# Kernel tuning notes

Measured on AMD Instinct MI355X. Metric: run time of the kernel, lower is better.

## Reference

```python
import jax, jax.numpy as jnp
import numpy as np

N_STATES = 32
N_CAMP = 64
DAYS = 365
BATCH = 128
BASIS = 1e-10


def setup_inputs() -> dict:
    key = jax.random.key(0)
    k1, k2, k3 = jax.random.split(key, 3)
    S = N_STATES
    adstock = jax.random.uniform(k1, (BATCH, N_CAMP, DAYS), dtype=jnp.float32)
    mu = jax.random.uniform(k2, ((S - 1) * (S - 1),), dtype=jnp.float32)
    beta = jax.random.uniform(k3, (N_CAMP * (S - 1) * (S - 1),), dtype=jnp.float32)
    return {"adstock": adstock, "mu": mu, "beta": beta}


def _transition(adstock, mu, beta):
    # adstock: [B, C, D]; time T = D - 1 (first day dropped, as in adstock[:, :, 1:])
    S = N_STATES
    B, C, D = adstock.shape
    T = D - 1
    # call() passes -mu into make_transition_matrix
    mu_m = jnp.reshape(-mu, (1, 1, S - 1, S - 1))
    beta_m = jnp.reshape(beta, (C, S - 1, S - 1))
    # tensordot(adstock[b, :, 1:], beta, [0, 0]) for every b -> einsum over camp axis
    O_beta = jnp.einsum('bct,cij->btij', adstock[:, :, 1:], beta_m)  # [B,T,S-1,S-1]
    num = jnp.exp(O_beta + mu_m)
    den = 1.0 + jnp.sum(num, axis=-1, keepdims=True)
    Q_div = num / den                          # [B,T,S-1,S-1] off-diagonal probs
    Q_same = 1.0 - jnp.sum(Q_div, axis=-1)     # [B,T,S-1]    stay probability
    # The TF diag-set loop places, for row i of Q_div: columns j<i stay at j,
    # columns j>=i shift to j+1, and Q_same goes on column i (insert-diagonal).
    i = jnp.arange(S - 1)[:, None]             # [S-1,1]
    j = jnp.arange(S)[None, :]                 # [1,S]
    idx = jnp.clip(jnp.where(j < i, j, j - 1), 0, S - 2)  # [S-1,S]
    gathered = jnp.take_along_axis(Q_div, jnp.broadcast_to(idx, (B, T, S - 1, S)), axis=-1)
    Q_temp = jnp.where(j == i, Q_same[..., None], gathered)  # [B,T,S-1,S]
    # Absorbing last row: basis everywhere, mass 1-(S-1)*basis on last state.
    last = jnp.full((B, T, 1, S), BASIS, dtype=adstock.dtype)
    last = last.at[..., -1].set(1.0 - (S - 1) * BASIS)
    Q = jnp.concatenate([Q_temp, last], axis=2)  # [B,T,S,S]
    return jnp.maximum(Q, BASIS)


def reference(adstock, mu, beta):
    return _transition(adstock, mu, beta)
```

## Files before the change

kernel.cpp:

```cpp
#include <hip/hip_runtime.h>
#include <cstdint>
#include <cstddef>

#define Bb 128
#define Cc 64
#define Dd 365
#define Tt 364
#define Ss 32
#define SM1 31
#define NIJ 961
#define BASISF 1e-10f
#define NBLK 256
#define NUNITS 11648
#define NWAVES 4096

typedef _Float16 f16x8 __attribute__((ext_vector_type(8)));
typedef float f32x4 __attribute__((ext_vector_type(4)));

__global__ void prep_kernel(const float* __restrict__ mu,
                            const float* __restrict__ beta,
                            _Float16* __restrict__ B2,
                            float* __restrict__ emu_perm) {
    int idx = blockIdx.x * blockDim.x + threadIdx.x;
    int m = idx >> 6, c = idx & 63;
    int rem = m & 255;
    int i = (m >> 8) * 8 + (rem >> 6) * 2 + ((rem & 15) >> 3);
    int j = 4 * (rem & 7) + ((rem >> 4) & 3);
    float val = (i < SM1 && j < SM1) ? beta[c * NIJ + i * SM1 + j] : 0.0f;
    B2[((size_t)(c >> 3) * 1024 + m) * 8 + (c & 7)] = (_Float16)val;
    if (idx < 1024) {
        int m2 = idx, rem2 = m2 & 255;
        int i2 = (m2 >> 8) * 8 + (rem2 >> 6) * 2 + ((rem2 & 15) >> 3);
        int j2 = 4 * (rem2 & 7) + ((rem2 >> 4) & 3);
        emu_perm[m2] = (i2 < SM1 && j2 < SM1) ? __expf(-mu[i2 * SM1 + j2]) : 1.0f;
    }
}

template <int CTRL>
__device__ __forceinline__ float dpp_mov(float x) {
    union { float f; int i; } u, v;
    u.f = x;
    v.i = __builtin_amdgcn_update_dpp(0, u.i, CTRL, 0xf, 0xf, true);
    return v.f;
}
template <int CTRL>
__device__ __forceinline__ float dpp_add(float s) { return s + dpp_mov<CTRL>(s); }

__global__ __launch_bounds__(1024, 1)
void transition_persist_kernel(const float* __restrict__ adstock,
                               const _Float16* __restrict__ B2,
                               const float* __restrict__ emu_perm,
                               float* __restrict__ out)
{
    const int tid  = threadIdx.x;
    const int lane = tid & 63;
    const int w    = tid >> 6;
    const int je   = lane & 15;
    const int grp  = lane >> 4;
    const int a     = je & 7;
    const int ihalf = je >> 3;
    const int j0    = 4 * a;

    __shared__ _Float16 Blds[65536];
    __shared__ float emuL[1024];

    #pragma unroll
    for (int s = 0; s < 8; ++s) {
        const int o8 = s * 8192 + tid * 8;
        *reinterpret_cast<f16x8*>(&Blds[o8]) =
            *reinterpret_cast<const f16x8*>(B2 + o8);
    }
    emuL[tid] = emu_perm[tid];
    __syncthreads();

    const float m3 = (a == 7) ? 0.0f : 1.0f;

    const int gw = blockIdx.x * 16 + w;
    const int ub = (int)(((long)NUNITS * gw) / NWAVES);
    const int ue = (int)(((long)NUNITS * (gw + 1)) / NWAVES);

    for (int u = ub; u < ue; ++u) {
        const int chunk = u >> 2;
        const int nq    = u & 3;
        const int bt0   = chunk * 16;

        const int bt = bt0 + je;
        const int b  = bt / Tt, t = bt - b * Tt;
        const float* abase = adstock + ((size_t)b * Cc) * Dd + 1 + t;

        float a0f[8], a1f[8];
        #pragma unroll
        for (int u8 = 0; u8 < 8; ++u8) {
            a0f[u8] = abase[(size_t)(grp * 8 + u8) * Dd];
            a1f[u8] = abase[(size_t)(32 + grp * 8 + u8) * Dd];
        }
        f16x8 a0, a1;
        #pragma unroll
        for (int u8 = 0; u8 < 8; ++u8) {
            a0[u8] = (_Float16)a0f[u8];
            a1[u8] = (_Float16)a1f[u8];
        }

        #pragma unroll
        for (int qp = 0; qp < 4; ++qp) {
            const int colb = nq * 256 + qp * 64 + je;
            f16x8 Bf[8];
            #pragma unroll
            for (int p = 0; p < 4; ++p) {
                Bf[2 * p]     = *reinterpret_cast<const f16x8*>(
                    &Blds[((0 * 4 + grp) * 1024 + colb + p * 16) * 8]);
                Bf[2 * p + 1] = *reinterpret_cast<const f16x8*>(
                    &Blds[((1 * 4 + grp) * 1024 + colb + p * 16) * 8]);
            }

            float emq[4];
            #pragma unroll
            for (int p = 0; p < 4; ++p)
                emq[p] = emuL[nq * 256 + qp * 64 + p * 16 + je];

            f32x4 acc[4];
            #pragma unroll
            for (int p = 0; p < 4; ++p) {
                f32x4 z = {0.f, 0.f, 0.f, 0.f};
                f32x4 t0 = __builtin_amdgcn_mfma_f32_16x16x32_f16(a0, Bf[2 * p], z, 0, 0, 0);
                acc[p] = __builtin_amdgcn_mfma_f32_16x16x32_f16(a1, Bf[2 * p + 1], t0, 0, 0, 0);
            }

            const int i_lane = nq * 8 + 2 * qp + ihalf;
            const size_t obase = (size_t)(bt0 + grp * 4) * 1024
                               + (size_t)i_lane * 32 + j0;

            #pragma unroll
            for (int r = 0; r < 4; ++r) {
                float np[4];
                #pragma unroll
                for (int p = 0; p < 4; ++p) np[p] = __expf(acc[p][r]) * emq[p];

                float s = np[0] + np[1] + fmaf(np[3], m3, np[2]);
                s = dpp_add<0xB1>(s);
                s = dpp_add<0x4E>(s);
                float t1 = dpp_mov<0x124>(s);
                float t2 = dpp_mov<0x12C>(s);
                s += (je & 4) ? t1 : t2;
                const float inv = __builtin_amdgcn_rcpf(1.0f + s);

                const float sh0 = dpp_mov<0x111>(np[3]);
                const float prev[4] = {sh0, np[0], np[1], np[2]};

                float v[4];
                #pragma unroll
                for (int p = 0; p < 4; ++p) {
                    const int j = j0 + p;
                    float x = (j < i_lane) ? np[p] * inv
                            : ((j == i_lane) ? inv : prev[p] * inv);
                    v[p] = fmaxf(x, BASISF);
                }
                if (nq == 3 && qp == 3) {
                    const bool ab = (i_lane == SM1);
                    v[0] = ab ? BASISF : v[0];
                    v[1] = ab ? BASISF : v[1];
                    v[2] = ab ? BASISF : v[2];
                    v[3] = ab ? ((a == 7) ? (1.0f - SM1 * BASISF) : BASISF) : v[3];
                }
                f32x4 vv = {v[0], v[1], v[2], v[3]};
                *reinterpret_cast<f32x4*>(out + obase + (size_t)r * 1024) = vv;
            }
        }
    }
}

__global__ __launch_bounds__(256, 4)
void transition_fallback_kernel(const float* __restrict__ adstock,
                                const float* __restrict__ beta,
                                const float* __restrict__ mu,
                                float* __restrict__ out) {
    const int b  = blockIdx.x;
    const int t0 = blockIdx.y * 16;
    const int tid = threadIdx.x;

    __shared__ float adT[Cc][16];
    __shared__ float num_lds[8][964];

    for (int k = tid; k < Cc * 16; k += 256) {
        int c = k >> 4, tt = k & 15, t = t0 + tt;
        adT[c][tt] = (t < Tt) ? adstock[(size_t)b * (Cc * Dd) + c * Dd + 1 + t] : 0.0f;
    }
    __syncthreads();

    const int ij0 = tid * 4;
    const bool active = (ij0 < 964);
    float acc[16][4];
    #pragma unroll
    for (int tt = 0; tt < 16; ++tt) { acc[tt][0]=0;acc[tt][1]=0;acc[tt][2]=0;acc[tt][3]=0; }

    if (active) {
        for (int c = 0; c < Cc; ++c) {
            const float* bsrc = beta + (size_t)c * NIJ;
            float w0 = (ij0+0<NIJ)?bsrc[ij0+0]:0.f, w1 = (ij0+1<NIJ)?bsrc[ij0+1]:0.f;
            float w2 = (ij0+2<NIJ)?bsrc[ij0+2]:0.f, w3 = (ij0+3<NIJ)?bsrc[ij0+3]:0.f;
            #pragma unroll
            for (int tt = 0; tt < 16; ++tt) {
                float av = adT[c][tt];
                acc[tt][0] = fmaf(av, w0, acc[tt][0]);
                acc[tt][1] = fmaf(av, w1, acc[tt][1]);
                acc[tt][2] = fmaf(av, w2, acc[tt][2]);
                acc[tt][3] = fmaf(av, w3, acc[tt][3]);
            }
        }
    }
    float m0=0,m1=0,m2=0,m3=0;
    if (active) {
        m0 = (ij0+0<NIJ)?mu[ij0+0]:0.f; m1 = (ij0+1<NIJ)?mu[ij0+1]:0.f;
        m2 = (ij0+2<NIJ)?mu[ij0+2]:0.f; m3 = (ij0+3<NIJ)?mu[ij0+3]:0.f;
    }
    const int q8 = tid >> 5, irow = tid & 31;
    #pragma unroll
    for (int half = 0; half < 2; ++half) {
        if (active) {
            #pragma unroll
            for (int q = 0; q < 8; ++q) {
                const int tt = half * 8 + q;
                num_lds[q][ij0+0] = __expf(acc[tt][0] - m0);
                num_lds[q][ij0+1] = __expf(acc[tt][1] - m1);
                num_lds[q][ij0+2] = __expf(acc[tt][2] - m2);
                num_lds[q][ij0+3] = __expf(acc[tt][3] - m3);
            }
        }
        __syncthreads();
        const int t = t0 + half * 8 + q8;
        if (t < Tt) {
            float* op = out + (((size_t)b * Tt + t) * Ss + irow) * Ss;
            if (irow < SM1) {
                float row[SM1]; float den = 1.0f;
                #pragma unroll
                for (int j = 0; j < SM1; ++j) { row[j] = num_lds[q8][irow*SM1+j]; den += row[j]; }
                const float inv = 1.0f / den;
                #pragma unroll
                for (int j = 0; j < Ss; ++j) {
                    float vv = (j < irow) ? row[j]*inv : ((j == irow) ? inv
                              : (j-1 < SM1 ? row[j-1]*inv : 0.f));
                    op[j] = fmaxf(vv, BASISF);
                }
            } else {
                #pragma unroll
                for (int j = 0; j < Ss; ++j) op[j] = (j == SM1) ? (1.0f - SM1*BASISF) : BASISF;
            }
        }
        __syncthreads();
    }
}

extern "C" void kernel_launch(void* const* d_in, const int* in_sizes, int n_in,
                              void* d_out, int out_size, void* d_ws, size_t ws_size,
                              hipStream_t stream) {
    const float* adstock = (const float*)d_in[0];
    const float* mu      = (const float*)d_in[1];
    const float* beta    = (const float*)d_in[2];
    float* out = (float*)d_out;

    const size_t need = (size_t)65536 * sizeof(_Float16) + 1024 * sizeof(float);

    if (ws_size >= need) {
        _Float16* B2 = (_Float16*)d_ws;
        float* emu_perm = (float*)((char*)d_ws + (size_t)65536 * sizeof(_Float16));
        prep_kernel<<<(1024 * Cc) / 256, 256, 0, stream>>>(mu, beta, B2, emu_perm);
        transition_persist_kernel<<<NBLK, 1024, 0, stream>>>(adstock, B2, emu_perm, out);
    } else {
        dim3 grid(Bb, (Tt + 15) / 16);
        transition_fallback_kernel<<<grid, 256, 0, stream>>>(adstock, beta, mu, out);
    }
}
```

Before: 48.35 us.

## Assign one whole 16-row chunk per wave and prefetch adstock before LDS fill

```diff
diff --git a/kernel.cpp b/kernel.cpp
--- a/kernel.cpp
+++ b/kernel.cpp
@@ -10,9 +10,9 @@
 #define SM1 31
 #define NIJ 961
 #define BASISF 1e-10f
+#define NUNIT 2912
 #define NBLK 256
-#define NUNITS 11648
-#define NWAVES 4096
+#define NWPB 12
 
 typedef _Float16 f16x8 __attribute__((ext_vector_type(8)));
 typedef float f32x4 __attribute__((ext_vector_type(4)));
@@ -46,11 +46,11 @@
 template <int CTRL>
 __device__ __forceinline__ float dpp_add(float s) { return s + dpp_mov<CTRL>(s); }
 
-__global__ __launch_bounds__(1024, 1)
-void transition_persist_kernel(const float* __restrict__ adstock,
-                               const _Float16* __restrict__ B2,
-                               const float* __restrict__ emu_perm,
-                               float* __restrict__ out)
+__global__ __launch_bounds__(768, 1)
+void transition_wave_kernel(const float* __restrict__ adstock,
+                            const _Float16* __restrict__ B2,
+                            const float* __restrict__ emu_perm,
+                            float* __restrict__ out)
 {
     const int tid  = threadIdx.x;
     const int lane = tid & 63;
@@ -64,46 +64,46 @@
     __shared__ _Float16 Blds[65536];
     __shared__ float emuL[1024];
 
-    #pragma unroll
-    for (int s = 0; s < 8; ++s) {
-        const int o8 = s * 8192 + tid * 8;
-        *reinterpret_cast<f16x8*>(&Blds[o8]) =
-            *reinterpret_cast<const f16x8*>(B2 + o8);
-    }
-    emuL[tid] = emu_perm[tid];
-    __syncthreads();
-
-    const float m3 = (a == 7) ? 0.0f : 1.0f;
-
-    const int gw = blockIdx.x * 16 + w;
-    const int ub = (int)(((long)NUNITS * gw) / NWAVES);
-    const int ue = (int)(((long)NUNITS * (gw + 1)) / NWAVES);
-
-    for (int u = ub; u < ue; ++u) {
-        const int chunk = u >> 2;
-        const int nq    = u & 3;
-        const int bt0   = chunk * 16;
-
-        const int bt = bt0 + je;
-        const int b  = bt / Tt, t = bt - b * Tt;
+    const int ub = (NUNIT * blockIdx.x) / NBLK;
+    const int ue = (NUNIT * (blockIdx.x + 1)) / NBLK;
+    const int unit = ub + w;
+    const bool active = (unit < ue);
+
+    float a0f[8], a1f[8];
+    if (active) {
+        const int bt = unit * 16 + je;
+        const int b = bt / Tt, t = bt - b * Tt;
         const float* abase = adstock + ((size_t)b * Cc) * Dd + 1 + t;
-
-        float a0f[8], a1f[8];
         #pragma unroll
         for (int u8 = 0; u8 < 8; ++u8) {
             a0f[u8] = abase[(size_t)(grp * 8 + u8) * Dd];
             a1f[u8] = abase[(size_t)(32 + grp * 8 + u8) * Dd];
         }
-        f16x8 a0, a1;
-        #pragma unroll
-        for (int u8 = 0; u8 < 8; ++u8) {
-            a0[u8] = (_Float16)a0f[u8];
-            a1[u8] = (_Float16)a1f[u8];
-        }
-
+    }
+
+    for (int o8 = tid * 8; o8 < 65536; o8 += 768 * 8) {
+        *reinterpret_cast<f16x8*>(&Blds[o8]) =
+            *reinterpret_cast<const f16x8*>(B2 + o8);
+    }
+    for (int e = tid; e < 1024; e += 768) emuL[e] = emu_perm[e];
+    __syncthreads();
+    if (!active) return;
+
+    f16x8 a0, a1;
+    #pragma unroll
+    for (int u8 = 0; u8 < 8; ++u8) {
+        a0[u8] = (_Float16)a0f[u8];
+        a1[u8] = (_Float16)a1f[u8];
+    }
+
+    const float m3 = (a == 7) ? 0.0f : 1.0f;
+    const int bt0 = unit * 16;
+    const size_t rowb = (size_t)(bt0 + grp * 4) * 1024 + j0;
+
+    for (int qq = 0; qq < 4; ++qq) {
         #pragma unroll
         for (int qp = 0; qp < 4; ++qp) {
-            const int colb = nq * 256 + qp * 64 + je;
+            const int colb = qq * 256 + qp * 64 + je;
             f16x8 Bf[8];
             #pragma unroll
             for (int p = 0; p < 4; ++p) {
@@ -116,7 +116,7 @@
             float emq[4];
             #pragma unroll
             for (int p = 0; p < 4; ++p)
-                emq[p] = emuL[nq * 256 + qp * 64 + p * 16 + je];
+                emq[p] = emuL[qq * 256 + qp * 64 + p * 16 + je];
 
             f32x4 acc[4];
             #pragma unroll
@@ -126,9 +126,8 @@
                 acc[p] = __builtin_amdgcn_mfma_f32_16x16x32_f16(a1, Bf[2 * p + 1], t0, 0, 0, 0);
             }
 
-            const int i_lane = nq * 8 + 2 * qp + ihalf;
-            const size_t obase = (size_t)(bt0 + grp * 4) * 1024
-                               + (size_t)i_lane * 32 + j0;
+            const int i_lane = qq * 8 + 2 * qp + ihalf;
+            const size_t obase = rowb + (size_t)i_lane * 32;
 
             #pragma unroll
             for (int r = 0; r < 4; ++r) {
@@ -155,7 +154,7 @@
                             : ((j == i_lane) ? inv : prev[p] * inv);
                     v[p] = fmaxf(x, BASISF);
                 }
-                if (nq == 3 && qp == 3) {
+                if (qq == 3 && qp == 3) {
                     const bool ab = (i_lane == SM1);
                     v[0] = ab ? BASISF : v[0];
                     v[1] = ab ? BASISF : v[1];
@@ -264,7 +263,7 @@
         _Float16* B2 = (_Float16*)d_ws;
         float* emu_perm = (float*)((char*)d_ws + (size_t)65536 * sizeof(_Float16));
         prep_kernel<<<(1024 * Cc) / 256, 256, 0, stream>>>(mu, beta, B2, emu_perm);
-        transition_persist_kernel<<<NBLK, 1024, 0, stream>>>(adstock, B2, emu_perm, out);
+        transition_wave_kernel<<<NBLK, 768, 0, stream>>>(adstock, B2, emu_perm, out);
     } else {
         dim3 grid(Bb, (Tt + 15) / 16);
         transition_fallback_kernel<<<grid, 256, 0, stream>>>(adstock, beta, mu, out);
```

After: 47.81 us. About the same (-1.1%).
